# Optimization experiments

Hardware: AMD Instinct MI355X
Metric: run time of the kernel (lower is better)

The kernel has to match this reference:

```python
import jax, jax.numpy as jnp
import numpy as np

B, N, D, E, DFF, CAP = 8, 2048, 1024, 8, 4096, 320


def setup_inputs() -> dict:
    key = jax.random.key(0)
    k1, k2, k3, k4 = jax.random.split(key, 4)
    return {
        "token_inputs": jax.random.normal(k1, (B, N, D), dtype=jnp.float32),
        "Wg": jax.random.normal(k2, (D, E), dtype=jnp.float32) * 0.02,
        "W1": jax.random.normal(k3, (E, D, DFF), dtype=jnp.float32) * 0.02,
        "W2": jax.random.normal(k4, (E, DFF, D), dtype=jnp.float32) * 0.02,
        "capacity": CAP,
    }


def _switch_route(token_inputs, Wg, capacity):
    # Top-1 switch routing -> dispatch one-hot [B,N,E,C], combine = dispatch * gate prob.
    logits = jnp.einsum('bnd,de->bne', token_inputs, Wg)
    probs = jax.nn.softmax(logits, axis=-1)
    gate = jnp.max(probs, axis=-1)                      # [B,N]
    expert_idx = jnp.argmax(probs, axis=-1)             # [B,N]
    mask = jax.nn.one_hot(expert_idx, probs.shape[-1], dtype=probs.dtype)  # [B,N,E]
    # 1-indexed position of each token within its chosen expert's queue
    pos = jnp.cumsum(mask, axis=1) * mask               # [B,N,E]
    mask = mask * (pos <= capacity)                     # drop tokens over capacity
    slot = (pos - 1.0).astype(jnp.int32)                # -1 where unrouted -> one_hot zeros
    dispatch = jax.nn.one_hot(slot, capacity, dtype=probs.dtype) * mask[..., None]  # [B,N,E,C]
    combine = dispatch * gate[:, :, None, None]
    return dispatch, combine


def reference(token_inputs, Wg, W1, W2, capacity):
    dispatch, combine = _switch_route(token_inputs, Wg, capacity)
    # Dispatch tokens to expert buffers: [B,E,C,D]
    expert_inputs = jnp.einsum('bnd,bnec->becd', token_inputs, dispatch)
    # Per-expert 2-layer relu FFN (grouped GEMM over E)
    h = jax.nn.relu(jnp.einsum('becd,edh->bech', expert_inputs, W1))
    expert_outputs = jnp.einsum('bech,ehd->becd', h, W2)
    # Combine back to token order, weighted by gate prob
    return jnp.einsum('becd,bnec->bnd', expert_outputs, combine)
```

## Files before the change

### kernel.cpp

```cpp
#include <hip/hip_runtime.h>

#define Bq 8
#define Nq 2048
#define Dq 1024
#define Eq 8
#define DFFq 4096
#define CAPq 320
#define Mq (Bq * CAPq)
#define Tq (Bq * Nq)

typedef __attribute__((ext_vector_type(8))) short bf16x8;
typedef __attribute__((ext_vector_type(4))) float f32x4;

static __device__ __forceinline__ unsigned short f2bf(float f) {
    union { float f; unsigned u; } v;
    v.f = f;
    unsigned r = v.u + 0x7fffu + ((v.u >> 16) & 1u);
    return (unsigned short)(r >> 16);
}

static __device__ __forceinline__ void gload_lds16(const void* g, void* l) {
    __builtin_amdgcn_global_load_lds(
        (const __attribute__((address_space(1))) unsigned int*)g,
        (__attribute__((address_space(3))) unsigned int*)l, 16, 0, 0);
}

__global__ __launch_bounds__(256) void route_kernel(
    const float* __restrict__ tok, const float* __restrict__ Wg,
    int* __restrict__ eidx, float* __restrict__ gate)
{
    int wv = threadIdx.x >> 6, lane = threadIdx.x & 63;
    int t = blockIdx.x * 4 + wv;
    const float* tp = tok + (size_t)t * Dq;
    float acc[8] = {0.f,0.f,0.f,0.f,0.f,0.f,0.f,0.f};
    for (int it = 0; it < Dq / 64; ++it) {
        int d = it * 64 + lane;
        float x = tp[d];
        const float4* w = (const float4*)(Wg + (size_t)d * 8);
        float4 w0 = w[0], w1 = w[1];
        acc[0] += x * w0.x; acc[1] += x * w0.y; acc[2] += x * w0.z; acc[3] += x * w0.w;
        acc[4] += x * w1.x; acc[5] += x * w1.y; acc[6] += x * w1.z; acc[7] += x * w1.w;
    }
#pragma unroll
    for (int e = 0; e < 8; ++e)
#pragma unroll
        for (int off = 32; off; off >>= 1)
            acc[e] += __shfl_xor(acc[e], off, 64);
    if (lane == 0) {
        float m = acc[0]; int bi = 0;
#pragma unroll
        for (int e = 1; e < 8; ++e) if (acc[e] > m) { m = acc[e]; bi = e; }
        float s = 0.f;
#pragma unroll
        for (int e = 0; e < 8; ++e) s += expf(acc[e] - m);
        eidx[t] = bi;
        gate[t] = 1.0f / s;
    }
}

__global__ __launch_bounds__(64) void slot_kernel(
    const int* __restrict__ eidx, int* __restrict__ tfs)
{
    int b = blockIdx.x >> 3, e = blockIdx.x & 7;
    int lane = threadIdx.x;
    const int* ip = eidx + (size_t)b * Nq;
    int base = (e * Bq + b) * CAPq;
    int cnt = 0;
    for (int it = 0; it < Nq / 64; ++it) {
        int n = it * 64 + lane;
        bool my = (ip[n] == e);
        unsigned long long mask = __ballot(my);
        if (my) {
            int pos = cnt + __popcll(mask & ((1ull << lane) - 1ull));
            if (pos < CAPq) tfs[base + pos] = b * Nq + n;
        }
        cnt += __popcll(mask);
    }
}

__global__ __launch_bounds__(128) void dispatch_kernel(
    const float* __restrict__ tok, const int* __restrict__ tfs,
    unsigned short* __restrict__ X)
{
    int r = blockIdx.x;
    int t = tfs[r];
    int d0 = threadIdx.x * 8;
    unsigned short o[8];
    if (t < 0) {
#pragma unroll
        for (int k = 0; k < 8; ++k) o[k] = 0;
    } else {
        const float4* p = (const float4*)(tok + (size_t)t * Dq + d0);
        float4 a = p[0], b = p[1];
        o[0]=f2bf(a.x); o[1]=f2bf(a.y); o[2]=f2bf(a.z); o[3]=f2bf(a.w);
        o[4]=f2bf(b.x); o[5]=f2bf(b.y); o[6]=f2bf(b.z); o[7]=f2bf(b.w);
    }
    *(uint4*)(X + (size_t)r * Dq + d0) = *(const uint4*)o;
}

__global__ __launch_bounds__(256) void transpose_cvt(
    const float* __restrict__ in, unsigned short* __restrict__ out,
    int R, int C)
{
    __shared__ float tile[32][33];
    int e = blockIdx.z;
    int c0 = blockIdx.x * 32, r0 = blockIdx.y * 32;
    int tx = threadIdx.x & 31, ty = threadIdx.x >> 5;
    const float* ip = in + (size_t)e * R * C;
#pragma unroll
    for (int rr = 0; rr < 4; ++rr)
        tile[ty + rr * 8][tx] = ip[(size_t)(r0 + ty + rr * 8) * C + c0 + tx];
    __syncthreads();
    unsigned short* op = out + (size_t)e * R * C;
#pragma unroll
    for (int rr = 0; rr < 4; ++rr)
        op[(size_t)(c0 + ty + rr * 8) * R + r0 + tx] = f2bf(tile[tx][ty + rr * 8]);
}

template <int MODE>
__global__ __launch_bounds__(256) void gemm_nt(
    const unsigned short* __restrict__ A,
    const unsigned short* __restrict__ Bt,
    unsigned short* __restrict__ Hout,
    float* __restrict__ Out,
    const int* __restrict__ tfs,
    const float* __restrict__ gate,
    int M, int N, int K)
{
    __shared__ __align__(16) unsigned short As[128 * 64];
    __shared__ __align__(16) unsigned short Bs[128 * 64];
    __shared__ int   t_lds[128];
    __shared__ float g_lds[128];

    const int tid = threadIdx.x;
    const int e  = blockIdx.z;
    const int n0 = blockIdx.x * 128;
    const int m0 = blockIdx.y * 128;
    const unsigned short* Ae = A  + (size_t)e * M * K + (size_t)m0 * K;
    const unsigned short* Be = Bt + (size_t)e * N * K + (size_t)n0 * K;

    if (MODE == 1 && tid < 128) {
        int t = tfs[e * M + m0 + tid];
        t_lds[tid] = t;
        g_lds[tid] = (t >= 0) ? gate[t] : 0.f;
    }

    const int lane = tid & 63;
    const int wv = tid >> 6;
    const int wr = wv >> 1, wc = wv & 1;
    const int lrow = lane & 15;
    const int lk = lane >> 4;
    const int swz = (lrow & 7) << 4;

    const int srow = tid >> 3;
    const int skb  = ((tid & 7) << 4) ^ (((tid >> 3) & 7) << 4);
    const int ldst = (tid >> 6) << 10;

    f32x4 acc[4][4] = {};

    for (int kt = 0; kt < K; kt += 64) {
        __syncthreads();
        const char* ga = (const char*)Ae + ((size_t)srow * K + kt) * 2 + skb;
        const char* gb = (const char*)Be + ((size_t)srow * K + kt) * 2 + skb;
#pragma unroll
        for (int inst = 0; inst < 4; ++inst) {
            gload_lds16(ga + (size_t)(inst * 32) * K * 2, (char*)As + inst * 4096 + ldst);
            gload_lds16(gb + (size_t)(inst * 32) * K * 2, (char*)Bs + inst * 4096 + ldst);
        }
        __syncthreads();
#pragma unroll
        for (int kk = 0; kk < 2; ++kk) {
            bf16x8 af[4], bfr[4];
#pragma unroll
            for (int i = 0; i < 4; ++i) {
                int row = wr * 64 + i * 16 + lrow;
                int addr = row * 128 + ((kk * 64 + lk * 16) ^ swz);
                af[i] = *(const bf16x8*)((const char*)As + addr);
            }
#pragma unroll
            for (int j = 0; j < 4; ++j) {
                int row = wc * 64 + j * 16 + lrow;
                int addr = row * 128 + ((kk * 64 + lk * 16) ^ swz);
                bfr[j] = *(const bf16x8*)((const char*)Bs + addr);
            }
#pragma unroll
            for (int i = 0; i < 4; ++i)
#pragma unroll
                for (int j = 0; j < 4; ++j)
                    acc[i][j] = __builtin_amdgcn_mfma_f32_16x16x32_bf16(
                        af[i], bfr[j], acc[i][j], 0, 0, 0);
        }
    }

    if (MODE == 0) {
        unsigned short* Hp = Hout + (size_t)e * M * N;
#pragma unroll
        for (int i = 0; i < 4; ++i) {
            int row = m0 + wr * 64 + i * 16 + lk * 4;
#pragma unroll
            for (int j = 0; j < 4; ++j) {
                int col = n0 + wc * 64 + j * 16 + lrow;
#pragma unroll
                for (int r = 0; r < 4; ++r)
                    Hp[(size_t)(row + r) * N + col] = f2bf(fmaxf(acc[i][j][r], 0.f));
            }
        }
    } else {
#pragma unroll
        for (int i = 0; i < 4; ++i) {
            int rowl = wr * 64 + i * 16 + lk * 4;
#pragma unroll
            for (int r = 0; r < 4; ++r) {
                int t = t_lds[rowl + r];
                if (t < 0) continue;
                float g = g_lds[rowl + r];
#pragma unroll
                for (int j = 0; j < 4; ++j) {
                    int col = n0 + wc * 64 + j * 16 + lrow;
                    Out[(size_t)t * Dq + col] = g * acc[i][j][r];
                }
            }
        }
    }
}

extern "C" void kernel_launch(void* const* d_in, const int* in_sizes, int n_in,
                              void* d_out, int out_size, void* d_ws, size_t ws_size,
                              hipStream_t stream)
{
    const float* tok = (const float*)d_in[0];
    const float* Wg  = (const float*)d_in[1];
    const float* W1  = (const float*)d_in[2];
    const float* W2  = (const float*)d_in[3];
    float* out = (float*)d_out;
    char* ws = (char*)d_ws;

    unsigned short* W1T = (unsigned short*)(ws);
    unsigned short* W2T = (unsigned short*)(ws + 67108864);
    unsigned short* X   = (unsigned short*)(ws + 134217728);
    unsigned short* H   = (unsigned short*)(ws + 176160768);
    int*   tfs  = (int*)(ws + 343932928);
    int*   eidx = (int*)(ws + 344014848);
    float* gate = (float*)(ws + 344080384);

    hipMemsetAsync(d_out, 0, (size_t)out_size * 4, stream);
    hipMemsetAsync(tfs, 0xFF, Eq * Mq * 4, stream);

    route_kernel<<<Tq / 4, 256, 0, stream>>>(tok, Wg, eidx, gate);
    slot_kernel<<<Bq * Eq, 64, 0, stream>>>(eidx, tfs);
    dispatch_kernel<<<Eq * Mq, 128, 0, stream>>>(tok, tfs, X);
    transpose_cvt<<<dim3(DFFq / 32, Dq / 32, Eq), 256, 0, stream>>>(W1, W1T, Dq, DFFq);
    transpose_cvt<<<dim3(Dq / 32, DFFq / 32, Eq), 256, 0, stream>>>(W2, W2T, DFFq, Dq);

    gemm_nt<0><<<dim3(DFFq / 128, Mq / 128, Eq), 256, 0, stream>>>(
        X, W1T, H, nullptr, nullptr, nullptr, Mq, DFFq, Dq);
    gemm_nt<1><<<dim3(Dq / 128, Mq / 128, Eq), 256, 0, stream>>>(
        H, W2T, nullptr, out, tfs, gate, Mq, Dq, DFFq);
}
```

Baseline: 584.4 us.

## Rewrite expert GEMMs with 256x128 tiles, triple-buffered LDS pipeline, and grid swizzle

Replaces the single-buffered 128x128 GEMM with a 512-thread, 256x128-tile kernel. It prefetches K tiles two steps ahead into a three-stage LDS ring, using fine-grained vmcnt waits instead of double __syncthreads, and raises MFMA wave priority. A flattened grid index is remapped so consecutive workgroups spread across XCD-like groups of eight. The aim is to hide global-load latency and improve operand reuse, at the cost of much larger LDS use (about 144 KB) and lower occupancy.

```diff
diff --git a/kernel.cpp b/kernel.cpp
--- a/kernel.cpp
+++ b/kernel.cpp
@@ -117,30 +117,38 @@
         op[(size_t)(c0 + ty + rr * 8) * R + r0 + tx] = f2bf(tile[tx][ty + rr * 8]);
 }
 
-template <int MODE>
-__global__ __launch_bounds__(256) void gemm_nt(
+template <int MODE, int Ndim, int Kdim>
+__global__ __launch_bounds__(512) void gemm3(
     const unsigned short* __restrict__ A,
     const unsigned short* __restrict__ Bt,
     unsigned short* __restrict__ Hout,
     float* __restrict__ Out,
     const int* __restrict__ tfs,
-    const float* __restrict__ gate,
-    int M, int N, int K)
-{
-    __shared__ __align__(16) unsigned short As[128 * 64];
-    __shared__ __align__(16) unsigned short Bs[128 * 64];
-    __shared__ int   t_lds[128];
-    __shared__ float g_lds[128];
+    const float* __restrict__ gate)
+{
+    constexpr int NT  = Kdim / 64;
+    constexpr int NTB = Ndim / 128;
+    constexpr int MT  = Mq / 256;
+    constexpr int NWG = MT * NTB * Eq;
+
+    __shared__ __align__(16) unsigned short As[3 * 256 * 64];
+    __shared__ __align__(16) unsigned short Bs[3 * 128 * 64];
+    __shared__ int   t_lds[256];
+    __shared__ float g_lds[256];
+
+    int flat = blockIdx.x;
+    int wg = (flat & 7) * (NWG / 8) + (flat >> 3);
+    int e   = wg / (MT * NTB);
+    int rem = wg - e * (MT * NTB);
+    int mb = rem / NTB, nb = rem - mb * NTB;
+    int m0 = mb * 256, n0 = nb * 128;
+
+    const unsigned short* Ae = A  + (size_t)e * Mq * Kdim + (size_t)m0 * Kdim;
+    const unsigned short* Be = Bt + (size_t)e * Ndim * Kdim + (size_t)n0 * Kdim;
 
     const int tid = threadIdx.x;
-    const int e  = blockIdx.z;
-    const int n0 = blockIdx.x * 128;
-    const int m0 = blockIdx.y * 128;
-    const unsigned short* Ae = A  + (size_t)e * M * K + (size_t)m0 * K;
-    const unsigned short* Be = Bt + (size_t)e * N * K + (size_t)n0 * K;
-
-    if (MODE == 1 && tid < 128) {
-        int t = tfs[e * M + m0 + tid];
+    if (MODE == 1 && tid < 256) {
+        int t = tfs[e * Mq + m0 + tid];
         t_lds[tid] = t;
         g_lds[tid] = (t >= 0) ? gate[t] : 0.f;
     }
@@ -153,75 +161,127 @@
     const int swz = (lrow & 7) << 4;
 
     const int srow = tid >> 3;
-    const int skb  = ((tid & 7) << 4) ^ (((tid >> 3) & 7) << 4);
-    const int ldst = (tid >> 6) << 10;
+    const int sk   = ((tid & 7) << 4) ^ (((tid >> 3) & 7) << 4);
+    const int wbase = wv << 10;
+
+    const char* gAb = (const char*)Ae + (size_t)srow * Kdim * 2 + sk;
+    const char* gBb = (const char*)Be + (size_t)srow * Kdim * 2 + sk;
+
+    #define STAGE_A(kt, buf)                                                    \
+        {   const char* _g = gAb + (size_t)(kt) * 2;                            \
+            char* _l = (char*)As + (buf) * 32768 + wbase;                       \
+            gload_lds16(_g,                         _l);                        \
+            gload_lds16(_g + (size_t) 64 * Kdim * 2, _l + 8192);                \
+            gload_lds16(_g + (size_t)128 * Kdim * 2, _l + 16384);               \
+            gload_lds16(_g + (size_t)192 * Kdim * 2, _l + 24576);  }
+    #define STAGE_B(kt, buf)                                                    \
+        {   const char* _g = gBb + (size_t)(kt) * 2;                            \
+            char* _l = (char*)Bs + (buf) * 16384 + wbase;                       \
+            gload_lds16(_g,                         _l);                        \
+            gload_lds16(_g + (size_t) 64 * Kdim * 2, _l + 8192);  }
 
     f32x4 acc[4][4] = {};
 
-    for (int kt = 0; kt < K; kt += 64) {
-        __syncthreads();
-        const char* ga = (const char*)Ae + ((size_t)srow * K + kt) * 2 + skb;
-        const char* gb = (const char*)Be + ((size_t)srow * K + kt) * 2 + skb;
-#pragma unroll
-        for (int inst = 0; inst < 4; ++inst) {
-            gload_lds16(ga + (size_t)(inst * 32) * K * 2, (char*)As + inst * 4096 + ldst);
-            gload_lds16(gb + (size_t)(inst * 32) * K * 2, (char*)Bs + inst * 4096 + ldst);
+    STAGE_A(0, 0);  STAGE_B(0, 0);
+    STAGE_A(64, 1); STAGE_B(64, 1);
+    asm volatile("s_waitcnt lgkmcnt(0)");
+    asm volatile("s_waitcnt vmcnt(6)");
+    __builtin_amdgcn_s_barrier();
+    __builtin_amdgcn_sched_barrier(0);
+
+    int cur = 0;
+    for (int t = 0; t < NT; ++t) {
+        const char* pa = (const char*)As + cur * 32768;
+        const char* pb = (const char*)Bs + cur * 16384;
+        int sbuf = cur + 2; if (sbuf >= 3) sbuf -= 3;
+        const int kt2 = (t + 2) * 64;
+        const bool st = (t + 2) < NT;
+
+        if (st) STAGE_A(kt2, sbuf);
+        bf16x8 af[4][2], bf0[2][2];
+#pragma unroll
+        for (int i = 0; i < 4; ++i)
+#pragma unroll
+            for (int kk = 0; kk < 2; ++kk)
+                af[i][kk] = *(const bf16x8*)(pa + (wr * 64 + i * 16 + lrow) * 128
+                                               + ((kk * 64 + lk * 16) ^ swz));
+#pragma unroll
+        for (int j = 0; j < 2; ++j)
+#pragma unroll
+            for (int kk = 0; kk < 2; ++kk)
+                bf0[j][kk] = *(const bf16x8*)(pb + (wc * 64 + j * 16 + lrow) * 128
+                                                + ((kk * 64 + lk * 16) ^ swz));
+        __builtin_amdgcn_s_setprio(1);
+#pragma unroll
+        for (int i = 0; i < 4; ++i)
+#pragma unroll
+            for (int j = 0; j < 2; ++j)
+#pragma unroll
+                for (int kk = 0; kk < 2; ++kk)
+                    acc[i][j] = __builtin_amdgcn_mfma_f32_16x16x32_bf16(
+                        af[i][kk], bf0[j][kk], acc[i][j], 0, 0, 0);
+        __builtin_amdgcn_s_setprio(0);
+
+        if (st) STAGE_B(kt2, sbuf);
+        bf16x8 bf1[2][2];
+#pragma unroll
+        for (int j = 0; j < 2; ++j)
+#pragma unroll
+            for (int kk = 0; kk < 2; ++kk)
+                bf1[j][kk] = *(const bf16x8*)(pb + (wc * 64 + (j + 2) * 16 + lrow) * 128
+                                                + ((kk * 64 + lk * 16) ^ swz));
+        __builtin_amdgcn_s_setprio(1);
+#pragma unroll
+        for (int i = 0; i < 4; ++i)
+#pragma unroll
+            for (int j = 0; j < 2; ++j)
+#pragma unroll
+                for (int kk = 0; kk < 2; ++kk)
+                    acc[i][j + 2] = __builtin_amdgcn_mfma_f32_16x16x32_bf16(
+                        af[i][kk], bf1[j][kk], acc[i][j + 2], 0, 0, 0);
+        __builtin_amdgcn_s_setprio(0);
+
+        if (st)                 asm volatile("s_waitcnt vmcnt(6)");
+        else if (t + 1 < NT)    asm volatile("s_waitcnt vmcnt(0)");
+        if (t + 1 < NT) {
+            __builtin_amdgcn_s_barrier();
+            __builtin_amdgcn_sched_barrier(0);
         }
-        __syncthreads();
-#pragma unroll
-        for (int kk = 0; kk < 2; ++kk) {
-            bf16x8 af[4], bfr[4];
-#pragma unroll
-            for (int i = 0; i < 4; ++i) {
-                int row = wr * 64 + i * 16 + lrow;
-                int addr = row * 128 + ((kk * 64 + lk * 16) ^ swz);
-                af[i] = *(const bf16x8*)((const char*)As + addr);
-            }
-#pragma unroll
-            for (int j = 0; j < 4; ++j) {
-                int row = wc * 64 + j * 16 + lrow;
-                int addr = row * 128 + ((kk * 64 + lk * 16) ^ swz);
-                bfr[j] = *(const bf16x8*)((const char*)Bs + addr);
-            }
-#pragma unroll
-            for (int i = 0; i < 4; ++i)
-#pragma unroll
-                for (int j = 0; j < 4; ++j)
-                    acc[i][j] = __builtin_amdgcn_mfma_f32_16x16x32_bf16(
-                        af[i], bfr[j], acc[i][j], 0, 0, 0);
-        }
+        cur = cur + 1; if (cur == 3) cur = 0;
     }
 
     if (MODE == 0) {
-        unsigned short* Hp = Hout + (size_t)e * M * N;
+        unsigned short* Hp = Hout + (size_t)e * Mq * Ndim;
 #pragma unroll
         for (int i = 0; i < 4; ++i) {
-            int row = m0 + wr * 64 + i * 16 + lk * 4;
+            int r0 = m0 + wr * 64 + i * 16 + lk * 4;
 #pragma unroll
             for (int j = 0; j < 4; ++j) {
                 int col = n0 + wc * 64 + j * 16 + lrow;
 #pragma unroll
                 for (int r = 0; r < 4; ++r)
-                    Hp[(size_t)(row + r) * N + col] = f2bf(fmaxf(acc[i][j][r], 0.f));
+                    Hp[(size_t)(r0 + r) * Ndim + col] = f2bf(fmaxf(acc[i][j][r], 0.f));
             }
         }
     } else {
 #pragma unroll
         for (int i = 0; i < 4; ++i) {
-            int rowl = wr * 64 + i * 16 + lk * 4;
+            int rl = wr * 64 + i * 16 + lk * 4;
 #pragma unroll
             for (int r = 0; r < 4; ++r) {
-                int t = t_lds[rowl + r];
-                if (t < 0) continue;
-                float g = g_lds[rowl + r];
+                int tt = t_lds[rl + r];
+                if (tt < 0) continue;
+                float g = g_lds[rl + r];
 #pragma unroll
                 for (int j = 0; j < 4; ++j) {
                     int col = n0 + wc * 64 + j * 16 + lrow;
-                    Out[(size_t)t * Dq + col] = g * acc[i][j][r];
+                    Out[(size_t)tt * Dq + col] = g * acc[i][j][r];
                 }
             }
         }
     }
+    #undef STAGE_A
+    #undef STAGE_B
 }
 
 extern "C" void kernel_launch(void* const* d_in, const int* in_sizes, int n_in,
@@ -252,8 +312,8 @@
     transpose_cvt<<<dim3(DFFq / 32, Dq / 32, Eq), 256, 0, stream>>>(W1, W1T, Dq, DFFq);
     transpose_cvt<<<dim3(Dq / 32, DFFq / 32, Eq), 256, 0, stream>>>(W2, W2T, DFFq, Dq);
 
-    gemm_nt<0><<<dim3(DFFq / 128, Mq / 128, Eq), 256, 0, stream>>>(
-        X, W1T, H, nullptr, nullptr, nullptr, Mq, DFFq, Dq);
-    gemm_nt<1><<<dim3(Dq / 128, Mq / 128, Eq), 256, 0, stream>>>(
-        H, W2T, nullptr, out, tfs, gate, Mq, Dq, DFFq);
-}
+    gemm3<0, DFFq, Dq><<<(Mq / 256) * (DFFq / 128) * Eq, 512, 0, stream>>>(
+        X, W1T, H, nullptr, nullptr, nullptr);
+    gemm3<1, Dq, DFFq><<<(Mq / 256) * (Dq / 128) * Eq, 512, 0, stream>>>(
+        H, W2T, nullptr, out, tfs, gate);
+}
```

Result: slower. 731.1 us (+25.1%).

## Rewrite expert GEMMs as 256x256 8-wave double-buffered ping-pong pipeline

Applied to the files above, without the earlier changes.

Replaces the 128x128 single-buffered grouped GEMM with a 256x256 tile, 512-thread kernel. It double-buffers LDS, interleaves global->LDS stages with MFMA phases separated by barriers and uses s_setprio. Workgroup IDs are remapped across XCDs, and dimensions become compile-time template parameters. This is meant to hide memory latency and improve operand reuse, at the cost of much larger LDS use (128KB), more registers and fragile hand-tuned waitcnt scheduling.

```diff
diff --git a/kernel.cpp b/kernel.cpp
--- a/kernel.cpp
+++ b/kernel.cpp
@@ -117,111 +117,194 @@
         op[(size_t)(c0 + ty + rr * 8) * R + r0 + tx] = f2bf(tile[tx][ty + rr * 8]);
 }
 
-template <int MODE>
-__global__ __launch_bounds__(256) void gemm_nt(
+template <int MODE, int Ndim, int Kdim>
+__global__ __launch_bounds__(512, 2) void gemm8p(
     const unsigned short* __restrict__ A,
     const unsigned short* __restrict__ Bt,
     unsigned short* __restrict__ Hout,
     float* __restrict__ Out,
     const int* __restrict__ tfs,
-    const float* __restrict__ gate,
-    int M, int N, int K)
-{
-    __shared__ __align__(16) unsigned short As[128 * 64];
-    __shared__ __align__(16) unsigned short Bs[128 * 64];
-    __shared__ int   t_lds[128];
-    __shared__ float g_lds[128];
+    const float* __restrict__ gate)
+{
+    constexpr int NKT = Kdim / 64;
+    constexpr int NI  = NKT / 2;
+    constexpr int NTB = Ndim / 256;
+    constexpr int MT  = Mq / 256;
+    constexpr int NWG = MT * NTB * Eq;
+
+    __shared__ __align__(16) unsigned short As[2 * 2 * 128 * 64];
+    __shared__ __align__(16) unsigned short Bs[2 * 2 * 128 * 64];
+    __shared__ int   t_lds[256];
+    __shared__ float g_lds[256];
+
+    int flat = blockIdx.x;
+    int wg = (flat & 7) * (NWG / 8) + (flat >> 3);
+    int e   = wg / (MT * NTB);
+    int rem = wg - e * (MT * NTB);
+    int mb = rem / NTB, nb = rem - mb * NTB;
+    int m0 = mb * 256, n0 = nb * 256;
+
+    const char* Ae = (const char*)(A  + (size_t)e * Mq * Kdim + (size_t)m0 * Kdim);
+    const char* Be = (const char*)(Bt + (size_t)e * Ndim * Kdim + (size_t)n0 * Kdim);
 
     const int tid = threadIdx.x;
-    const int e  = blockIdx.z;
-    const int n0 = blockIdx.x * 128;
-    const int m0 = blockIdx.y * 128;
-    const unsigned short* Ae = A  + (size_t)e * M * K + (size_t)m0 * K;
-    const unsigned short* Be = Bt + (size_t)e * N * K + (size_t)n0 * K;
-
-    if (MODE == 1 && tid < 128) {
-        int t = tfs[e * M + m0 + tid];
+    if (MODE == 1 && tid < 256) {
+        int t = tfs[e * Mq + m0 + tid];
         t_lds[tid] = t;
         g_lds[tid] = (t >= 0) ? gate[t] : 0.f;
     }
+    __syncthreads();
 
     const int lane = tid & 63;
     const int wv = tid >> 6;
-    const int wr = wv >> 1, wc = wv & 1;
+    const int wr = wv & 1, wc = wv >> 1;
     const int lrow = lane & 15;
     const int lk = lane >> 4;
-    const int swz = (lrow & 7) << 4;
-
-    const int srow = tid >> 3;
-    const int skb  = ((tid & 7) << 4) ^ (((tid >> 3) & 7) << 4);
-    const int ldst = (tid >> 6) << 10;
-
-    f32x4 acc[4][4] = {};
-
-    for (int kt = 0; kt < K; kt += 64) {
-        __syncthreads();
-        const char* ga = (const char*)Ae + ((size_t)srow * K + kt) * 2 + skb;
-        const char* gb = (const char*)Be + ((size_t)srow * K + kt) * 2 + skb;
-#pragma unroll
-        for (int inst = 0; inst < 4; ++inst) {
-            gload_lds16(ga + (size_t)(inst * 32) * K * 2, (char*)As + inst * 4096 + ldst);
-            gload_lds16(gb + (size_t)(inst * 32) * K * 2, (char*)Bs + inst * 4096 + ldst);
+    const int swz = (lane & 7) << 4;
+
+    const int sk = ((tid & 7) << 4) ^ (((tid >> 3) & 7) << 4);
+    const size_t Kb = (size_t)Kdim * 2;
+    const char* gA = Ae + (size_t)(tid >> 3) * Kb + sk;
+    const char* gB = Be + (size_t)(tid >> 3) * Kb + sk;
+    const int ldst = wv << 10;
+
+    #define STG(gbase, lds, buf, h, kt) {                                      \
+        const char* _g = (gbase) + (size_t)((h) * 128) * Kb + (size_t)(kt) * 128; \
+        char* _l = (char*)(lds) + ((buf) * 2 + (h)) * 16384 + ldst;             \
+        gload_lds16(_g,                   _l);                                  \
+        gload_lds16(_g + (size_t)64 * Kb, _l + 8192); }
+
+    bf16x8 aq[4][2];
+    bf16x8 bq[2][2][2];
+    f32x4  acc[2][2][4][2] = {};
+
+    #define LDA(buf, mi) {                                                      \
+        const char* _p = (const char*)As + ((buf) * 2 + (mi)) * 16384;          \
+        _Pragma("unroll")                                                       \
+        for (int i = 0; i < 4; ++i) {                                           \
+            int rh = wr * 64 + i * 16 + lrow;                                   \
+            aq[i][0] = *(const bf16x8*)(_p + rh * 128 + ((lk * 16) ^ swz));     \
+            aq[i][1] = *(const bf16x8*)(_p + rh * 128 + ((64 + lk * 16) ^ swz)); } }
+
+    #define LDB(buf, nj) {                                                      \
+        const char* _p = (const char*)Bs + ((buf) * 2 + (nj)) * 16384;          \
+        _Pragma("unroll")                                                       \
+        for (int j = 0; j < 2; ++j) {                                           \
+            int rh = wc * 32 + j * 16 + lrow;                                   \
+            bq[nj][j][0] = *(const bf16x8*)(_p + rh * 128 + ((lk * 16) ^ swz)); \
+            bq[nj][j][1] = *(const bf16x8*)(_p + rh * 128 + ((64 + lk * 16) ^ swz)); } }
+
+    #define MM(mi, nj)                                                          \
+        _Pragma("unroll")                                                       \
+        for (int i = 0; i < 4; ++i)                                             \
+        _Pragma("unroll")                                                       \
+        for (int j = 0; j < 2; ++j)                                             \
+        _Pragma("unroll")                                                       \
+        for (int kk = 0; kk < 2; ++kk)                                          \
+            acc[mi][nj][i][j] = __builtin_amdgcn_mfma_f32_16x16x32_bf16(        \
+                aq[i][kk], bq[nj][j][kk], acc[mi][nj][i][j], 0, 0, 0);
+
+    #define PH_BAR() { __builtin_amdgcn_s_barrier(); __builtin_amdgcn_sched_barrier(0); }
+    #define LGKM0()  { asm volatile("s_waitcnt lgkmcnt(0)"); __builtin_amdgcn_sched_barrier(0); }
+    #define PRIO_MM(mi, nj) { __builtin_amdgcn_s_setprio(1); MM(mi, nj); __builtin_amdgcn_s_setprio(0); }
+
+    STG(gA, As, 0, 0, 0);
+    STG(gB, Bs, 0, 0, 0);
+    STG(gA, As, 0, 1, 0);
+    STG(gB, Bs, 0, 1, 0);
+    STG(gA, As, 1, 0, 1);
+    STG(gB, Bs, 1, 0, 1);
+    asm volatile("s_waitcnt vmcnt(4)");
+    PH_BAR();
+
+    for (int u = 0; u < NI; ++u) {
+        const int kt0 = 2 * u, kt1 = 2 * u + 1;
+        const bool lastI = (u == NI - 1);
+
+        LDA(0, 0); LDB(0, 0);
+        STG(gA, As, 1, 1, kt1);
+        PH_BAR(); LGKM0(); PRIO_MM(0, 0); PH_BAR();
+
+        LDB(0, 1);
+        STG(gB, Bs, 1, 1, kt1);
+        PH_BAR(); LGKM0(); PRIO_MM(0, 1); PH_BAR();
+
+        LDA(0, 1);
+        if (!lastI) STG(gA, As, 0, 0, kt0 + 2);
+        PH_BAR(); LGKM0(); PRIO_MM(1, 0); PH_BAR();
+
+        if (!lastI) STG(gB, Bs, 0, 0, kt0 + 2);
+        PH_BAR(); LGKM0(); PRIO_MM(1, 1);
+        if (lastI) { asm volatile("s_waitcnt vmcnt(0)"); }
+        else       { asm volatile("s_waitcnt vmcnt(4)"); }
+        PH_BAR();
+
+        LDA(1, 0); LDB(1, 0);
+        if (!lastI) STG(gA, As, 0, 1, kt0 + 2);
+        PH_BAR(); LGKM0(); PRIO_MM(0, 0); PH_BAR();
+
+        LDB(1, 1);
+        if (!lastI) STG(gB, Bs, 0, 1, kt0 + 2);
+        PH_BAR(); LGKM0(); PRIO_MM(0, 1); PH_BAR();
+
+        LDA(1, 1);
+        if (!lastI) STG(gA, As, 1, 0, kt1 + 2);
+        PH_BAR(); LGKM0(); PRIO_MM(1, 0); PH_BAR();
+
+        if (!lastI) STG(gB, Bs, 1, 0, kt1 + 2);
+        PH_BAR(); LGKM0(); PRIO_MM(1, 1);
+        if (!lastI) {
+            asm volatile("s_waitcnt vmcnt(4)");
+            PH_BAR();
         }
-        __syncthreads();
-#pragma unroll
-        for (int kk = 0; kk < 2; ++kk) {
-            bf16x8 af[4], bfr[4];
-#pragma unroll
-            for (int i = 0; i < 4; ++i) {
-                int row = wr * 64 + i * 16 + lrow;
-                int addr = row * 128 + ((kk * 64 + lk * 16) ^ swz);
-                af[i] = *(const bf16x8*)((const char*)As + addr);
-            }
-#pragma unroll
-            for (int j = 0; j < 4; ++j) {
-                int row = wc * 64 + j * 16 + lrow;
-                int addr = row * 128 + ((kk * 64 + lk * 16) ^ swz);
-                bfr[j] = *(const bf16x8*)((const char*)Bs + addr);
-            }
-#pragma unroll
-            for (int i = 0; i < 4; ++i)
-#pragma unroll
-                for (int j = 0; j < 4; ++j)
-                    acc[i][j] = __builtin_amdgcn_mfma_f32_16x16x32_bf16(
-                        af[i], bfr[j], acc[i][j], 0, 0, 0);
-        }
     }
 
     if (MODE == 0) {
-        unsigned short* Hp = Hout + (size_t)e * M * N;
+        unsigned short* Hp = Hout + (size_t)e * Mq * Ndim;
+#pragma unroll
+        for (int mi = 0; mi < 2; ++mi)
+#pragma unroll
+        for (int nj = 0; nj < 2; ++nj)
 #pragma unroll
         for (int i = 0; i < 4; ++i) {
-            int row = m0 + wr * 64 + i * 16 + lk * 4;
-#pragma unroll
-            for (int j = 0; j < 4; ++j) {
-                int col = n0 + wc * 64 + j * 16 + lrow;
+            int row = m0 + mi * 128 + wr * 64 + i * 16 + lk * 4;
+#pragma unroll
+            for (int j = 0; j < 2; ++j) {
+                int col = n0 + nj * 128 + wc * 32 + j * 16 + lrow;
 #pragma unroll
                 for (int r = 0; r < 4; ++r)
-                    Hp[(size_t)(row + r) * N + col] = f2bf(fmaxf(acc[i][j][r], 0.f));
+                    Hp[(size_t)(row + r) * Ndim + col] =
+                        f2bf(fmaxf(acc[mi][nj][i][j][r], 0.f));
             }
         }
     } else {
 #pragma unroll
+        for (int mi = 0; mi < 2; ++mi)
+#pragma unroll
         for (int i = 0; i < 4; ++i) {
-            int rowl = wr * 64 + i * 16 + lk * 4;
+            int rl = mi * 128 + wr * 64 + i * 16 + lk * 4;
 #pragma unroll
             for (int r = 0; r < 4; ++r) {
-                int t = t_lds[rowl + r];
-                if (t < 0) continue;
-                float g = g_lds[rowl + r];
-#pragma unroll
-                for (int j = 0; j < 4; ++j) {
-                    int col = n0 + wc * 64 + j * 16 + lrow;
-                    Out[(size_t)t * Dq + col] = g * acc[i][j][r];
+                int tt = t_lds[rl + r];
+                if (tt < 0) continue;
+                float g = g_lds[rl + r];
+#pragma unroll
+                for (int nj = 0; nj < 2; ++nj)
+#pragma unroll
+                for (int j = 0; j < 2; ++j) {
+                    int col = n0 + nj * 128 + wc * 32 + j * 16 + lrow;
+                    Out[(size_t)tt * Dq + col] = g * acc[mi][nj][i][j][r];
                 }
             }
         }
     }
+    #undef STG
+    #undef LDA
+    #undef LDB
+    #undef MM
+    #undef PH_BAR
+    #undef LGKM0
+    #undef PRIO_MM
 }
 
 extern "C" void kernel_launch(void* const* d_in, const int* in_sizes, int n_in,
@@ -252,8 +335,8 @@
     transpose_cvt<<<dim3(DFFq / 32, Dq / 32, Eq), 256, 0, stream>>>(W1, W1T, Dq, DFFq);
     transpose_cvt<<<dim3(Dq / 32, DFFq / 32, Eq), 256, 0, stream>>>(W2, W2T, DFFq, Dq);
 
-    gemm_nt<0><<<dim3(DFFq / 128, Mq / 128, Eq), 256, 0, stream>>>(
-        X, W1T, H, nullptr, nullptr, nullptr, Mq, DFFq, Dq);
-    gemm_nt<1><<<dim3(Dq / 128, Mq / 128, Eq), 256, 0, stream>>>(
-        H, W2T, nullptr, out, tfs, gate, Mq, Dq, DFFq);
-}
+    gemm8p<0, DFFq, Dq><<<(Mq / 256) * (DFFq / 256) * Eq, 512, 0, stream>>>(
+        X, W1T, H, nullptr, nullptr, nullptr);
+    gemm8p<1, Dq, DFFq><<<(Mq / 256) * (Dq / 256) * Eq, 512, 0, stream>>>(
+        H, W2T, nullptr, out, tfs, gate);
+}
```

Result: faster. 572.8 us (-2.0%).

## Double-buffer GEMM LDS loads, remap workgroups per XCD, zero only dropped tokens

Applied to the files above, without the earlier changes.

The GEMM main loop now uses two LDS buffers. The loads for tile k+2 are issued while tile k is computed, with explicit waitcnt and barriers, and s_setprio is raised around the MFMA block. The grid is flattened and workgroups are remapped round-robin across the 8 XCDs so that neighbouring tiles share L2. The full output memset is replaced by having slot_kernel zero only the rows of tokens dropped for capacity. The changes double LDS use per block and add launch bounds of 2 blocks per SM. The vmcnt(0) wait placed right after issuing the next load may limit how much overlap the pipelining actually gets.

```diff
diff --git a/kernel.cpp b/kernel.cpp
--- a/kernel.cpp
+++ b/kernel.cpp
@@ -59,7 +59,8 @@
 }
 
 __global__ __launch_bounds__(64) void slot_kernel(
-    const int* __restrict__ eidx, int* __restrict__ tfs)
+    const int* __restrict__ eidx, int* __restrict__ tfs,
+    float* __restrict__ out)
 {
     int b = blockIdx.x >> 3, e = blockIdx.x & 7;
     int lane = threadIdx.x;
@@ -72,7 +73,13 @@
         unsigned long long mask = __ballot(my);
         if (my) {
             int pos = cnt + __popcll(mask & ((1ull << lane) - 1ull));
-            if (pos < CAPq) tfs[base + pos] = b * Nq + n;
+            if (pos < CAPq) {
+                tfs[base + pos] = b * Nq + n;
+            } else {
+                float4 z = {0.f, 0.f, 0.f, 0.f};
+                float4* op = (float4*)(out + (size_t)(b * Nq + n) * Dq);
+                for (int q = 0; q < Dq / 4; ++q) op[q] = z;
+            }
         }
         cnt += __popcll(mask);
     }
@@ -118,7 +125,7 @@
 }
 
 template <int MODE>
-__global__ __launch_bounds__(256) void gemm_nt(
+__global__ __launch_bounds__(256, 2) void gemm_nt(
     const unsigned short* __restrict__ A,
     const unsigned short* __restrict__ Bt,
     unsigned short* __restrict__ Hout,
@@ -127,22 +134,33 @@
     const float* __restrict__ gate,
     int M, int N, int K)
 {
-    __shared__ __align__(16) unsigned short As[128 * 64];
-    __shared__ __align__(16) unsigned short Bs[128 * 64];
+    __shared__ __align__(16) unsigned short As[2][128 * 64];
+    __shared__ __align__(16) unsigned short Bs[2][128 * 64];
     __shared__ int   t_lds[128];
     __shared__ float g_lds[128];
 
     const int tid = threadIdx.x;
-    const int e  = blockIdx.z;
-    const int n0 = blockIdx.x * 128;
-    const int m0 = blockIdx.y * 128;
+
+    const int NTB = N >> 7;
+    const int MT  = M >> 7;
+    const int nwg = MT * NTB * Eq;
+    int flat = blockIdx.x;
+    int wg = (flat & 7) * (nwg >> 3) + (flat >> 3);
+    int e   = wg / (MT * NTB);
+    int rem = wg - e * (MT * NTB);
+    int mb = rem / NTB, nb = rem - mb * NTB;
+    const int m0 = mb << 7, n0 = nb << 7;
+
     const unsigned short* Ae = A  + (size_t)e * M * K + (size_t)m0 * K;
     const unsigned short* Be = Bt + (size_t)e * N * K + (size_t)n0 * K;
 
-    if (MODE == 1 && tid < 128) {
-        int t = tfs[e * M + m0 + tid];
-        t_lds[tid] = t;
-        g_lds[tid] = (t >= 0) ? gate[t] : 0.f;
+    if (MODE == 1) {
+        if (tid < 128) {
+            int t = tfs[e * M + m0 + tid];
+            t_lds[tid] = t;
+            g_lds[tid] = (t >= 0) ? gate[t] : 0.f;
+        }
+        __syncthreads();
     }
 
     const int lane = tid & 63;
@@ -156,18 +174,33 @@
     const int skb  = ((tid & 7) << 4) ^ (((tid >> 3) & 7) << 4);
     const int ldst = (tid >> 6) << 10;
 
+    const char* gAb = (const char*)Ae + ((size_t)srow * K) * 2 + skb;
+    const char* gBb = (const char*)Be + ((size_t)srow * K) * 2 + skb;
+
+    #define STG(tile, buf) {                                                   \
+        const char* _ga = gAb + (size_t)(tile) * 128;                          \
+        const char* _gb = gBb + (size_t)(tile) * 128;                          \
+        char* _la = (char*)As + (buf) * 16384 + ldst;                          \
+        char* _lb = (char*)Bs + (buf) * 16384 + ldst;                          \
+        _Pragma("unroll")                                                      \
+        for (int _i = 0; _i < 4; ++_i) {                                       \
+            gload_lds16(_ga + (size_t)(_i * 32) * K * 2, _la + _i * 4096);     \
+            gload_lds16(_gb + (size_t)(_i * 32) * K * 2, _lb + _i * 4096);     \
+        } }
+
     f32x4 acc[4][4] = {};
-
-    for (int kt = 0; kt < K; kt += 64) {
-        __syncthreads();
-        const char* ga = (const char*)Ae + ((size_t)srow * K + kt) * 2 + skb;
-        const char* gb = (const char*)Be + ((size_t)srow * K + kt) * 2 + skb;
-#pragma unroll
-        for (int inst = 0; inst < 4; ++inst) {
-            gload_lds16(ga + (size_t)(inst * 32) * K * 2, (char*)As + inst * 4096 + ldst);
-            gload_lds16(gb + (size_t)(inst * 32) * K * 2, (char*)Bs + inst * 4096 + ldst);
-        }
-        __syncthreads();
+    const int NK = K >> 6;
+
+    STG(0, 0);
+    STG(1, 1);
+    asm volatile("s_waitcnt vmcnt(8)");
+    __builtin_amdgcn_s_barrier();
+    __builtin_amdgcn_sched_barrier(0);
+
+    for (int kt = 0; kt < NK; ++kt) {
+        const int buf = kt & 1;
+        const char* pa = (const char*)As + buf * 16384;
+        const char* pb = (const char*)Bs + buf * 16384;
 #pragma unroll
         for (int kk = 0; kk < 2; ++kk) {
             bf16x8 af[4], bfr[4];
@@ -175,20 +208,28 @@
             for (int i = 0; i < 4; ++i) {
                 int row = wr * 64 + i * 16 + lrow;
                 int addr = row * 128 + ((kk * 64 + lk * 16) ^ swz);
-                af[i] = *(const bf16x8*)((const char*)As + addr);
+                af[i] = *(const bf16x8*)(pa + addr);
             }
 #pragma unroll
             for (int j = 0; j < 4; ++j) {
                 int row = wc * 64 + j * 16 + lrow;
                 int addr = row * 128 + ((kk * 64 + lk * 16) ^ swz);
-                bfr[j] = *(const bf16x8*)((const char*)Bs + addr);
-            }
+                bfr[j] = *(const bf16x8*)(pb + addr);
+            }
+            __builtin_amdgcn_s_setprio(1);
 #pragma unroll
             for (int i = 0; i < 4; ++i)
 #pragma unroll
                 for (int j = 0; j < 4; ++j)
                     acc[i][j] = __builtin_amdgcn_mfma_f32_16x16x32_bf16(
                         af[i], bfr[j], acc[i][j], 0, 0, 0);
+            __builtin_amdgcn_s_setprio(0);
+        }
+        if (kt + 1 < NK) {
+            asm volatile("s_waitcnt vmcnt(0)");
+            __builtin_amdgcn_s_barrier();
+            __builtin_amdgcn_sched_barrier(0);
+            if (kt + 2 < NK) STG(kt + 2, buf);
         }
     }
 
@@ -222,6 +263,7 @@
             }
         }
     }
+    #undef STG
 }
 
 extern "C" void kernel_launch(void* const* d_in, const int* in_sizes, int n_in,
@@ -243,17 +285,16 @@
     int*   eidx = (int*)(ws + 344014848);
     float* gate = (float*)(ws + 344080384);
 
-    hipMemsetAsync(d_out, 0, (size_t)out_size * 4, stream);
     hipMemsetAsync(tfs, 0xFF, Eq * Mq * 4, stream);
 
     route_kernel<<<Tq / 4, 256, 0, stream>>>(tok, Wg, eidx, gate);
-    slot_kernel<<<Bq * Eq, 64, 0, stream>>>(eidx, tfs);
+    slot_kernel<<<Bq * Eq, 64, 0, stream>>>(eidx, tfs, out);
     dispatch_kernel<<<Eq * Mq, 128, 0, stream>>>(tok, tfs, X);
     transpose_cvt<<<dim3(DFFq / 32, Dq / 32, Eq), 256, 0, stream>>>(W1, W1T, Dq, DFFq);
     transpose_cvt<<<dim3(Dq / 32, DFFq / 32, Eq), 256, 0, stream>>>(W2, W2T, DFFq, Dq);
 
-    gemm_nt<0><<<dim3(DFFq / 128, Mq / 128, Eq), 256, 0, stream>>>(
+    gemm_nt<0><<<(Mq / 128) * (DFFq / 128) * Eq, 256, 0, stream>>>(
         X, W1T, H, nullptr, nullptr, nullptr, Mq, DFFq, Dq);
-    gemm_nt<1><<<dim3(Dq / 128, Mq / 128, Eq), 256, 0, stream>>>(
+    gemm_nt<1><<<(Mq / 128) * (Dq / 128) * Eq, 256, 0, stream>>>(
         H, W2T, nullptr, out, tfs, gate, Mq, Dq, DFFq);
 }
```

Result: slower. 659.0 us (+12.8%).
